# Performance work log

Hardware: AMD Instinct MI355X
Metric: run time of the kernel (lower is better)

Reference implementation:

```python
import jax, jax.numpy as jnp
import numpy as np

B, T, S, H, V, MAXL = 8, 128, 256, 1024, 32000, 512
STD = 0.02


def _ln(x, g, b):
    m = jnp.mean(x, -1, keepdims=True)
    v = jnp.mean((x - m) ** 2, -1, keepdims=True)
    return (x - m) / jnp.sqrt(v + 1e-5) * g + b


def setup_inputs() -> dict:
    key = jax.random.key(0)
    ks = jax.random.split(key, 16)
    n = lambda k, shape: jax.random.normal(k, shape, jnp.float32) * STD
    inp = {
        "input_ids": jax.random.randint(ks[0], (B, T), 0, V),
        "encoder_hidden_states": jax.random.normal(ks[1], (B, S, H), jnp.float32),
        "pattern_masks": jax.random.randint(ks[2], (B, T, V), 0, 2).astype(bool),
        "attention_mask": jnp.ones((B, S), bool),
        "tok_emb": n(ks[3], (V, H)),
        "pos_emb": n(ks[4], (MAXL, H)),
        "w_ih": n(ks[5], (4 * H, H)),
        "w_hh": n(ks[6], (4 * H, H)),
        "b_ih": jnp.zeros((4 * H,), jnp.float32),
        "b_hh": jnp.zeros((4 * H,), jnp.float32),
        "wq": n(ks[7], (H, H)), "bq": jnp.zeros((H,), jnp.float32),
        "wk": n(ks[8], (H, H)), "bk": jnp.zeros((H,), jnp.float32),
        "wc": n(ks[9], (H, 2 * H)), "bc": jnp.zeros((H,), jnp.float32),
        "wo": n(ks[10], (V, H)), "bo": jnp.zeros((V,), jnp.float32),
        "g1": n(ks[11], (H,)), "be1": jnp.zeros((H,), jnp.float32),
        "g2": n(ks[12], (H,)), "be2": jnp.zeros((H,), jnp.float32),
    }
    return inp


def reference(input_ids, encoder_hidden_states, pattern_masks, attention_mask,
              tok_emb, pos_emb, w_ih, w_hh, b_ih, b_hh,
              wq, bq, wk, bk, wc, bc, wo, bo, g1, be1, g2, be2):
    # Token + positional embedding (dropout is identity in eval)
    x = tok_emb[input_ids] + pos_emb[:T][None, :, :]  # [B,T,H]

    # Single-layer LSTM (PyTorch gate order i,f,g,o) via scan over time
    def step(carry, xt):
        h, c = carry
        gates = xt @ w_ih.T + b_ih + h @ w_hh.T + b_hh
        i, f, g, o = jnp.split(gates, 4, axis=-1)
        c = jax.nn.sigmoid(f) * c + jax.nn.sigmoid(i) * jnp.tanh(g)
        h = jax.nn.sigmoid(o) * jnp.tanh(c)
        return (h, c), h

    h0 = jnp.zeros((B, H), x.dtype)
    _, hs = jax.lax.scan(step, (h0, h0), jnp.swapaxes(x, 0, 1))
    lstm_out = jnp.swapaxes(hs, 0, 1)  # [B,T,H]

    # Attention: per-position loop in torch == batched over T (keys invariant)
    qn = _ln(lstm_out @ wq.T + bq, g1, be1)              # [B,T,H]
    kn = _ln(encoder_hidden_states @ wk.T + bk, g1, be1)  # [B,S,H]
    scale = H ** (-0.5) * 0.5
    scores = jnp.einsum('bth,bsh->bts', qn, kn) * scale
    am = attention_mask[:, None, :]
    scores = jnp.where(am, scores, -10000.0)
    mx = jnp.max(scores, -1, keepdims=True)
    ex = jnp.exp(scores - mx)
    ex = jnp.where(am, ex, 0.0)
    w = ex / (jnp.sum(ex, -1, keepdims=True) + 1e-6)
    ctx = jnp.einsum('bts,bsh->bth', w, kn)              # [B,T,H]

    hidden = _ln(jnp.concatenate([lstm_out, ctx], -1) @ wc.T + bc, g2, be2)
    logits = hidden @ wo.T + bo                           # [B,T,V]
    logits = jnp.where(pattern_masks, logits, -10000.0)
    return logits
```

## Files before the change

### kernel.cpp

```cpp
#include <hip/hip_runtime.h>
#include <cstdint>
#include <cstddef>

#define Bdim 8
#define Tdim 128
#define Sdim 256
#define Hdim 1024
#define Vdim 32000
#define SENT 0xFFFFFFFFFFFFFFFFULL

typedef unsigned short u16;
typedef unsigned long long u64;
typedef __attribute__((ext_vector_type(8))) short short8;
typedef __attribute__((ext_vector_type(4))) short short4v;
typedef __attribute__((ext_vector_type(4))) float f32x4;
typedef __attribute__((ext_vector_type(2))) unsigned long long u64x2;

union Frag { short8 v; short4v h[2]; };

__device__ __forceinline__ float bf2f(u16 u){
  union { unsigned int i; float f; } x; x.i = ((unsigned int)u) << 16; return x.f;
}
__device__ __forceinline__ u16 f2b(float f){
  union { float f; unsigned int u; } x; x.f = f;
  unsigned int r = x.u + 0x7FFFu + ((x.u >> 16) & 1u);
  return (u16)(r >> 16);
}
__device__ __forceinline__ float ftanh(float x){
  x = fminf(10.f, fmaxf(-10.f, x));
  const float e = __expf(2.f * x);
  return (e - 1.f) / (e + 1.f);
}

__device__ __forceinline__ void gload16(const void* g, void* l){
  __builtin_amdgcn_global_load_lds((const __attribute__((address_space(1))) unsigned int*)g,
                                   (__attribute__((address_space(3))) unsigned int*)l, 16, 0, 0);
}

__device__ __forceinline__ int qsw(int r){ return (r + (r >> 2)) & 3; }

__device__ __forceinline__ u64 aload(const u64* p){
  return __hip_atomic_load(p, __ATOMIC_RELAXED, __HIP_MEMORY_SCOPE_AGENT);
}
__device__ __forceinline__ void astore(u64* p, u64 v){
  __hip_atomic_store(p, v, __ATOMIC_RELAXED, __HIP_MEMORY_SCOPE_AGENT);
}

__global__ __launch_bounds__(256) void detect_bool_k(const unsigned char* __restrict__ p, int* __restrict__ flag){
  __shared__ int s;
  if (threadIdx.x == 0) s = 0;
  __syncthreads();
  int loc = 0;
  for (int i = threadIdx.x; i < 65536; i += 256)
    if ((i & 3) && p[i]) loc = 1;
  if (loc) atomicOr(&s, 1);
  __syncthreads();
  if (threadIdx.x == 0) flag[0] = s;
}

__device__ __forceinline__ bool mask_at(const void* m, size_t idx, int byteflag){
  if (byteflag) return ((const unsigned char*)m)[idx] != 0;
  return ((const int*)m)[idx] != 0;
}

template<typename OutT, bool BF32, int MASK>
__device__ __forceinline__ void gemm_core(
    char* ldsA0, char* ldsB0, char* ldsA1, char* ldsB1,
    int m0, int n0, int z,
    const u16* __restrict__ A, int lda, long sA,
    const void* __restrict__ Bp, int ldb, long sB,
    OutT* __restrict__ C, int ldc, long sC,
    const float* __restrict__ bias,
    const void* __restrict__ mask,
    const int* __restrict__ mflag,
    int K, float alpha)
{
  const int tid  = threadIdx.x;
  const int lane = tid & 63, wid = tid >> 6;
  const int lm = lane & 15, lg = lane >> 4;
  const int wm = wid >> 1, wn = wid & 1;
  const char* Ab = (const char*)(A + (size_t)z * sA);

  f32x4 acc[4][4];
#pragma unroll
  for (int i = 0; i < 4; i++)
#pragma unroll
    for (int j = 0; j < 4; j++) acc[i][j] = (f32x4){0.f, 0.f, 0.f, 0.f};

  const int brow = tid >> 1, bhalf = tid & 1;
  const int qb_st = qsw(brow);

  auto stageA = [&](char* dst, int k0){
    const char* ga = Ab + ((size_t)m0 * lda + k0) * 2;
    const int f0 = tid, f1 = tid + 256;
    const int r0 = f0 >> 2, r1 = f1 >> 2;
    gload16(ga + (size_t)r0 * (lda * 2) + ((f0 & 3) ^ qsw(r0)) * 16, dst + (f0 & ~63) * 16);
    gload16(ga + (size_t)r1 * (lda * 2) + ((f1 & 3) ^ qsw(r1)) * 16, dst + (f1 & ~63) * 16);
  };
  auto stageB16 = [&](char* dst, int k0){
    const char* gb = (const char*)((const u16*)Bp + (size_t)z * sB) + ((size_t)n0 * ldb + k0) * 2;
    const int f0 = tid, f1 = tid + 256;
    const int r0 = f0 >> 2, r1 = f1 >> 2;
    gload16(gb + (size_t)r0 * (ldb * 2) + ((f0 & 3) ^ qsw(r0)) * 16, dst + (f0 & ~63) * 16);
    gload16(gb + (size_t)r1 * (ldb * 2) + ((f1 & 3) ^ qsw(r1)) * 16, dst + (f1 & ~63) * 16);
  };

  float4 nv0, nv1, nv2, nv3;
  auto loadB32 = [&](int k0){
    const float* Bf = (const float*)Bp + (size_t)z * sB;
    const float4* src = (const float4*)(Bf + (size_t)(n0 + brow) * ldb + k0 + bhalf * 16);
    nv0 = src[0]; nv1 = src[1]; nv2 = src[2]; nv3 = src[3];
  };
  auto writeB32 = [&](char* dst){
    union { short8 v; short s[8]; } p0, p1;
    p0.s[0]=(short)f2b(nv0.x); p0.s[1]=(short)f2b(nv0.y); p0.s[2]=(short)f2b(nv0.z); p0.s[3]=(short)f2b(nv0.w);
    p0.s[4]=(short)f2b(nv1.x); p0.s[5]=(short)f2b(nv1.y); p0.s[6]=(short)f2b(nv1.z); p0.s[7]=(short)f2b(nv1.w);
    p1.s[0]=(short)f2b(nv2.x); p1.s[1]=(short)f2b(nv2.y); p1.s[2]=(short)f2b(nv2.z); p1.s[3]=(short)f2b(nv2.w);
    p1.s[4]=(short)f2b(nv3.x); p1.s[5]=(short)f2b(nv3.y); p1.s[6]=(short)f2b(nv3.z); p1.s[7]=(short)f2b(nv3.w);
    char* base = dst + brow * 64;
    *(short8*)(base + (((bhalf * 2 + 0) ^ qb_st) * 16)) = p0.v;
    *(short8*)(base + (((bhalf * 2 + 1) ^ qb_st) * 16)) = p1.v;
  };

  stageA(ldsA0, 0);
  if (BF32) { loadB32(0); writeB32(ldsB0); }
  else stageB16(ldsB0, 0);
  __syncthreads();

  char *cA = ldsA0, *cB = ldsB0, *nA = ldsA1, *nB = ldsB1;
  const int nk = K >> 5;
  for (int i = 0; i < nk; i++) {
    const bool more = (i + 1) < nk;
    if (more) {
      stageA(nA, (i + 1) << 5);
      if (BF32) loadB32((i + 1) << 5);
      else stageB16(nB, (i + 1) << 5);
    }
    Frag a[4], b[4];
#pragma unroll
    for (int mi = 0; mi < 4; mi++) {
      const int rr = wm * 64 + mi * 16 + lm;
      const int q = qsw(rr);
      const char* p = cA + rr * 64 + (lg & 1) * 8;
      a[mi].h[0] = *(const short4v*)(p + (((lg >> 1) ^ q) * 16));
      a[mi].h[1] = *(const short4v*)(p + ((((lg >> 1) | 2) ^ q) * 16));
    }
#pragma unroll
    for (int ni = 0; ni < 4; ni++) {
      const int rr = wn * 64 + ni * 16 + lm;
      const int q = qsw(rr);
      const char* p = cB + rr * 64 + (lg & 1) * 8;
      b[ni].h[0] = *(const short4v*)(p + (((lg >> 1) ^ q) * 16));
      b[ni].h[1] = *(const short4v*)(p + ((((lg >> 1) | 2) ^ q) * 16));
    }
#pragma unroll
    for (int mi = 0; mi < 4; mi++)
#pragma unroll
      for (int ni = 0; ni < 4; ni++)
        acc[mi][ni] = __builtin_amdgcn_mfma_f32_16x16x32_bf16(a[mi].v, b[ni].v, acc[mi][ni], 0, 0, 0);
    if (BF32 && more) writeB32(nB);
    __syncthreads();
    char* t;
    t = cA; cA = nA; nA = t;
    t = cB; cB = nB; nB = t;
  }

  const int bflag = (MASK == 1) ? *mflag : 0;
#pragma unroll
  for (int mi = 0; mi < 4; mi++) {
#pragma unroll
    for (int ni = 0; ni < 4; ni++) {
      const int row = m0 + wm * 64 + mi * 16 + lg * 4;
      const int col = n0 + wn * 64 + ni * 16 + lm;
      const float bb = bias ? bias[col] : 0.f;
#pragma unroll
      for (int j = 0; j < 4; j++) {
        float v = acc[mi][ni][j] * alpha + bb;
        const size_t midx = (size_t)(row + j) * ldc + col;
        if (MASK == 1) { if (!mask_at(mask, midx, bflag)) v = -10000.0f; }
        if (MASK == 2) { if (!((const unsigned char*)mask)[midx]) v = -10000.0f; }
        const size_t o = (size_t)z * sC + midx;
        if constexpr (sizeof(OutT) == 2) C[o] = (OutT)f2b(v); else C[o] = (OutT)v;
      }
    }
  }
}

template<typename OutT, bool BF32, int MASK, bool SWAP>
__global__ __launch_bounds__(256) void gemm_bt(
    const u16* __restrict__ A, int lda, long sA,
    const void* __restrict__ Bp, int ldb, long sB,
    OutT* __restrict__ C, int ldc, long sC,
    const float* __restrict__ bias,
    const void* __restrict__ mask,
    const int* __restrict__ mflag,
    int K, float alpha)
{
  __shared__ alignas(16) char lds[32768];
  const int m0 = (SWAP ? blockIdx.x : blockIdx.y) * 128;
  const int n0 = (SWAP ? blockIdx.y : blockIdx.x) * 128;
  gemm_core<OutT, BF32, MASK>(lds, lds + 8192, lds + 16384, lds + 24576,
      m0, n0, blockIdx.z, A, lda, sA, Bp, ldb, sB, C, ldc, sC,
      bias, mask, mflag, K, alpha);
}

__device__ void lstm_body(char* smem,
    const u16* __restrict__ xpre, const u16* __restrict__ whh,
    u16* __restrict__ hbuf, int bx)
{
  u16* wlds = (u16*)smem;
  u16* hlds = (u16*)(smem + 131072);
  float* g_lds = (float*)(smem + 147456);
  u16* hout = (u16*)(smem + 149632);
  const int tid = threadIdx.x, lane = tid & 63, wid = tid >> 6;
  const int lm = lane & 15, lg = lane >> 4;
  const int gcol0 = bx * 64;

  for (int q = tid; q < 8192; q += 256) {
    const int r = q >> 7, cc = q & 127;
    gload16(whh + (size_t)(gcol0 + r) * 1024 + (size_t)(cc ^ (r & 7)) * 8,
            (char*)wlds + (q & ~63) * 16);
  }

  float c_reg = 0.f;
  const int m_u = lane & 7, u_u = lane >> 3;
  const int rloc = wid * 16 + lm, swb = rloc & 7, swa = lm & 7;
  const u16* wl = wlds + rloc * 1024;
  const u16* hl = hlds + swa * 1024;
  const int gcol = gcol0 + wid * 16 + lm;
  const int pk = tid >> 2, qq = tid & 3;

  for (int t = 0; t < Tdim; t++) {
    u16 xv[4];
#pragma unroll
    for (int j = 0; j < 4; j++) {
      const int m = lg * 4 + j;
      xv[j] = (m < 8) ? xpre[(size_t)(m * Tdim + t) * 4096 + gcol] : (u16)0;
    }
    if (t > 0) {
      const u64* ps = (const u64*)(hbuf + ((size_t)(t - 1) * 64 + pk) * 128) + qq * 8;
      u64 w0=SENT,w1=SENT,w2=SENT,w3=SENT,w4=SENT,w5=SENT,w6=SENT,w7=SENT;
      for (;;) {
        if (w0 == SENT) w0 = aload(ps + 0);
        if (w1 == SENT) w1 = aload(ps + 1);
        if (w2 == SENT) w2 = aload(ps + 2);
        if (w3 == SENT) w3 = aload(ps + 3);
        if (w4 == SENT) w4 = aload(ps + 4);
        if (w5 == SENT) w5 = aload(ps + 5);
        if (w6 == SENT) w6 = aload(ps + 6);
        if (w7 == SENT) w7 = aload(ps + 7);
        if (w0 != SENT && w1 != SENT && w2 != SENT && w3 != SENT &&
            w4 != SENT && w5 != SENT && w6 != SENT && w7 != SENT) break;
        __builtin_amdgcn_s_sleep(1);
      }
      {
        const int m = qq * 2;
        u64x2 a; a[0] = w0; a[1] = w1;
        u64x2 b; b[0] = w2; b[1] = w3;
        *(u64x2*)((char*)hlds + m * 2048 + (((pk * 2 + 0) ^ m) * 16)) = a;
        *(u64x2*)((char*)hlds + m * 2048 + (((pk * 2 + 1) ^ m) * 16)) = b;
      }
      {
        const int m = qq * 2 + 1;
        u64x2 a; a[0] = w4; a[1] = w5;
        u64x2 b; b[0] = w6; b[1] = w7;
        *(u64x2*)((char*)hlds + m * 2048 + (((pk * 2 + 0) ^ m) * 16)) = a;
        *(u64x2*)((char*)hlds + m * 2048 + (((pk * 2 + 1) ^ m) * 16)) = b;
      }
    }
    __syncthreads();

    f32x4 acc;
#pragma unroll
    for (int j = 0; j < 4; j++) acc[j] = bf2f(xv[j]);

    if (t > 0) {
#pragma unroll 4
      for (int kk = 0; kk < 32; kk++) {
        const int c0 = kk * 4 + (lg >> 1);
        const int sub = (lg & 1) * 4;
        Frag a, b;
        a.h[0] = *(const short4v*)(hl + ((c0 ^ swa) << 3) + sub);
        a.h[1] = *(const short4v*)(hl + (((c0 + 2) ^ swa) << 3) + sub);
        b.h[0] = *(const short4v*)(wl + ((c0 ^ swb) << 3) + sub);
        b.h[1] = *(const short4v*)(wl + (((c0 + 2) ^ swb) << 3) + sub);
        acc = __builtin_amdgcn_mfma_f32_16x16x32_bf16(a.v, b.v, acc, 0, 0, 0);
      }
    }
#pragma unroll
    for (int j = 0; j < 4; j++) {
      const int m = lg * 4 + j;
      if (m < 8) g_lds[(wid * 8 + m) * 17 + lm] = acc[j];
    }
    __syncthreads();
    if (lane < 32) {
      const float gi = g_lds[(wid * 8 + m_u) * 17 + u_u * 4 + 0];
      const float gf = g_lds[(wid * 8 + m_u) * 17 + u_u * 4 + 1];
      const float gg = g_lds[(wid * 8 + m_u) * 17 + u_u * 4 + 2];
      const float go = g_lds[(wid * 8 + m_u) * 17 + u_u * 4 + 3];
      const float si = 1.f / (1.f + __expf(-gi));
      const float sf = 1.f / (1.f + __expf(-gf));
      const float so = 1.f / (1.f + __expf(-go));
      const float cn = sf * c_reg + si * ftanh(gg);
      c_reg = cn;
      const float hn = so * ftanh(cn);
      hout[m_u * 16 + wid * 4 + u_u] = f2b(hn);
    }
    __syncthreads();
    if (tid < 16) {
      const int m = tid >> 1, half = tid & 1;
      const u64* src = (const u64*)(hout + m * 16 + half * 8);
      u64* dst = (u64*)(hbuf + ((size_t)t * 64 + bx) * 128 + m * 16 + half * 8);
      astore(dst, src[0]);
      astore(dst + 1, src[1]);
    }
  }
}

__global__ __launch_bounds__(256) void lstm_plus(
    const u16* __restrict__ xpre, const u16* __restrict__ whh,
    u16* __restrict__ hbuf,
    const u16* __restrict__ encb, const u16* __restrict__ wkb,
    float* __restrict__ klin, const float* __restrict__ bk,
    const float* __restrict__ wo, u16* __restrict__ wob,
    const void* __restrict__ pmask, unsigned char* __restrict__ pmaskb,
    const int* __restrict__ bflag)
{
  __shared__ alignas(16) char smem[149888];
  const int bx = blockIdx.x;
  if (bx < 64) {
    lstm_body(smem, xpre, whh, hbuf, bx);
  } else if (bx < 192) {
    const int idx = bx - 64;
    gemm_core<float, false, 0>(smem, smem + 8192, smem + 16384, smem + 24576,
        (idx >> 3) * 128, (idx & 7) * 128, 0,
        encb, 1024, 0, wkb, 1024, 0, klin, 1024, 0, bk, nullptr, nullptr, 1024, 1.f);
  } else {
    const int s = bx - 192;
    const int tid = threadIdx.x;
    if (wob) {
      for (int r = s; r < Vdim; r += 64) {
        const size_t i = (size_t)r * 1024 + tid * 4;
        const float4 v = *(const float4*)(wo + i);
        u16* op = wob + i;
        op[0] = f2b(v.x); op[1] = f2b(v.y); op[2] = f2b(v.z); op[3] = f2b(v.w);
      }
    }
    if (pmaskb) {
      const int bfl = *bflag;
      const size_t total = (size_t)Bdim * Tdim * Vdim;
      const size_t nthr = 64 * 256;
      if (bfl == 0) {
        for (size_t i = ((size_t)s * 256 + tid) * 4; i < total; i += nthr * 4) {
          const int4 v = *(const int4*)((const int*)pmask + i);
          uchar4 o;
          o.x = v.x ? 1 : 0; o.y = v.y ? 1 : 0; o.z = v.z ? 1 : 0; o.w = v.w ? 1 : 0;
          *(uchar4*)(pmaskb + i) = o;
        }
      } else {
        for (size_t i = ((size_t)s * 256 + tid) * 16; i < total; i += nthr * 16) {
          *(int4*)(pmaskb + i) = *(const int4*)((const unsigned char*)pmask + i);
        }
      }
    }
  }
}

__global__ __launch_bounds__(256) void hbuf_cat_k(const u16* __restrict__ hbuf, u16* __restrict__ cat){
  const int t = blockIdx.x, tid = threadIdx.x;
  const int p = tid >> 2, q = tid & 3;
  const u64* src = (const u64*)(hbuf + ((size_t)t * 64 + p) * 128);
#pragma unroll
  for (int m = 0; m < 8; m++) {
    const u64 v = src[m * 4 + q];
    *(u64*)(cat + (size_t)(m * Tdim + t) * 2048 + p * 16 + q * 4) = v;
  }
}

__global__ __launch_bounds__(256) void prep_k(
    const float* __restrict__ w_hh, const float* __restrict__ w_ih,
    const float* __restrict__ wq,   const float* __restrict__ wk,
    const float* __restrict__ wc,   const float* __restrict__ enc,
    const int* __restrict__ ids,
    const float* __restrict__ tok,  const float* __restrict__ pos,
    const float* __restrict__ b_ih, const float* __restrict__ b_hh,
    u16* __restrict__ whhb, u16* __restrict__ wihb,
    u16* __restrict__ wqb,  u16* __restrict__ wkb,  u16* __restrict__ wcb,
    u16* __restrict__ encb, u16* __restrict__ xbf,
    float* __restrict__ biasf, u64* __restrict__ hbuf)
{
  const int b = blockIdx.x, tid = threadIdx.x;
  if (b < 8192) {
    const bool ih = b >= 4096;
    const int r = b & 4095;
    const int p = (r & 3) * Hdim + (r >> 2);
    const float4 v = *(const float4*)((ih ? w_ih : w_hh) + (size_t)p * Hdim + tid * 4);
    u16* op = (ih ? wihb : whhb) + (size_t)r * Hdim + tid * 4;
    op[0] = f2b(v.x); op[1] = f2b(v.y); op[2] = f2b(v.z); op[3] = f2b(v.w);
  } else if (b < 9216) {
    const size_t i = (size_t)(b - 8192) * 1024 + tid * 4;
    const float4 v = *(const float4*)(wq + i);
    u16* op = wqb + i;
    op[0] = f2b(v.x); op[1] = f2b(v.y); op[2] = f2b(v.z); op[3] = f2b(v.w);
  } else if (b < 10240) {
    const size_t i = (size_t)(b - 9216) * 1024 + tid * 4;
    const float4 v = *(const float4*)(wk + i);
    u16* op = wkb + i;
    op[0] = f2b(v.x); op[1] = f2b(v.y); op[2] = f2b(v.z); op[3] = f2b(v.w);
  } else if (b < 12288) {
    const size_t i = (size_t)(b - 10240) * 1024 + tid * 4;
    const float4 v = *(const float4*)(wc + i);
    u16* op = wcb + i;
    op[0] = f2b(v.x); op[1] = f2b(v.y); op[2] = f2b(v.z); op[3] = f2b(v.w);
  } else if (b < 14336) {
    const size_t i = (size_t)(b - 12288) * 1024 + tid * 4;
    const float4 v = *(const float4*)(enc + i);
    u16* op = encb + i;
    op[0] = f2b(v.x); op[1] = f2b(v.y); op[2] = f2b(v.z); op[3] = f2b(v.w);
  } else if (b < 15360) {
    const int row = b - 14336;
    const int t = row & (Tdim - 1);
    const int id = ids[row];
    const int h0 = tid * 4;
    const float4 a = *(const float4*)(tok + (size_t)id * Hdim + h0);
    const float4 p = *(const float4*)(pos + (size_t)t * Hdim + h0);
    u16* op = xbf + (size_t)row * Hdim + h0;
    op[0] = f2b(a.x + p.x); op[1] = f2b(a.y + p.y); op[2] = f2b(a.z + p.z); op[3] = f2b(a.w + p.w);
  } else if (b < 15364) {
    const int n0 = (b - 15360) * 1024 + tid * 4;
#pragma unroll
    for (int j = 0; j < 4; j++) {
      const int n = n0 + j;
      const int p = (n & 3) * Hdim + (n >> 2);
      biasf[n] = b_ih[p] + b_hh[p];
    }
  } else {
    const size_t i = ((size_t)(b - 15364) * 256 + tid) * 4;
    u64x2 s2; s2[0] = SENT; s2[1] = SENT;
    *(u64x2*)(hbuf + i)     = s2;
    *(u64x2*)(hbuf + i + 2) = s2;
  }
}

__global__ __launch_bounds__(256) void ln_rows(const float* __restrict__ in, u16* __restrict__ out,
                                               const float* __restrict__ g, const float* __restrict__ be){
  const int row = blockIdx.x, tid = threadIdx.x;
  const int lane = tid & 63, wid = tid >> 6;
  const float4 x = *(const float4*)(in + (size_t)row * Hdim + tid * 4);
  float s = x.x + x.y + x.z + x.w;
  float q = x.x * x.x + x.y * x.y + x.z * x.z + x.w * x.w;
  for (int o = 32; o; o >>= 1) { s += __shfl_down(s, o, 64); q += __shfl_down(q, o, 64); }
  __shared__ float sm[8];
  if (lane == 0) { sm[wid] = s; sm[4 + wid] = q; }
  __syncthreads();
  const float ts = sm[0] + sm[1] + sm[2] + sm[3];
  const float tq = sm[4] + sm[5] + sm[6] + sm[7];
  const float mean = ts * (1.f / Hdim);
  const float var  = tq * (1.f / Hdim) - mean * mean;
  const float r = rsqrtf(var + 1e-5f);
  const int h0 = tid * 4;
  const float4 gv = *(const float4*)(g + h0);
  const float4 bv = *(const float4*)(be + h0);
  u16* op = out + (size_t)row * Hdim + h0;
  op[0] = f2b((x.x - mean) * r * gv.x + bv.x);
  op[1] = f2b((x.y - mean) * r * gv.y + bv.y);
  op[2] = f2b((x.z - mean) * r * gv.z + bv.z);
  op[3] = f2b((x.w - mean) * r * gv.w + bv.w);
}
__global__ __launch_bounds__(256) void softmax_k(const float* __restrict__ sc, const void* __restrict__ am,
                                                 const int* __restrict__ mflag, u16* __restrict__ w){
  const int row = blockIdx.x, tid = threadIdx.x;
  const int lane = tid & 63, wid = tid >> 6;
  const int b = row >> 7;
  const int bflag = *mflag;
  const float v = sc[(size_t)row * Sdim + tid];
  const bool mk = mask_at(am, (size_t)b * Sdim + tid, bflag);
  const float vm = mk ? v : -10000.0f;
  float mx = vm;
  for (int o = 32; o; o >>= 1) mx = fmaxf(mx, __shfl_down(mx, o, 64));
  __shared__ float sm[8];
  if (lane == 0) sm[wid] = mx;
  __syncthreads();
  mx = fmaxf(fmaxf(sm[0], sm[1]), fmaxf(sm[2], sm[3]));
  const float ex = mk ? expf(vm - mx) : 0.f;
  float ss = ex;
  for (int o = 32; o; o >>= 1) ss += __shfl_down(ss, o, 64);
  if (lane == 0) sm[4 + wid] = ss;
  __syncthreads();
  const float tot = sm[4] + sm[5] + sm[6] + sm[7];
  w[(size_t)row * Sdim + tid] = f2b(ex / (tot + 1e-6f));
}
__global__ __launch_bounds__(256) void transp_k(const u16* __restrict__ kn, u16* __restrict__ knT){
  __shared__ u16 tile[64][65];
  const int b = blockIdx.z, h0 = blockIdx.x * 64, s0 = blockIdx.y * 64;
  const u16* src = kn  + (size_t)b * Sdim * Hdim;
  u16* dst       = knT + (size_t)b * Hdim * Sdim;
  for (int e = threadIdx.x; e < 4096; e += 256) {
    const int r = e >> 6, c = e & 63;
    tile[r][c] = src[(size_t)(s0 + r) * Hdim + h0 + c];
  }
  __syncthreads();
  for (int e = threadIdx.x; e < 4096; e += 256) {
    const int hr = e >> 6, scc = e & 63;
    dst[(size_t)(h0 + hr) * Sdim + s0 + scc] = tile[scc][hr];
  }
}

extern "C" void kernel_launch(void* const* d_in, const int* in_sizes, int n_in,
                              void* d_out, int out_size, void* d_ws, size_t ws_size,
                              hipStream_t stream) {
  const int*   input_ids = (const int*)d_in[0];
  const float* enc   = (const float*)d_in[1];
  const void*  pmask = d_in[2];
  const void*  amask = d_in[3];
  const float* tok  = (const float*)d_in[4];
  const float* pos  = (const float*)d_in[5];
  const float* w_ih = (const float*)d_in[6];
  const float* w_hh = (const float*)d_in[7];
  const float* b_ih = (const float*)d_in[8];
  const float* b_hh = (const float*)d_in[9];
  const float* wq = (const float*)d_in[10];
  const float* bq = (const float*)d_in[11];
  const float* wk = (const float*)d_in[12];
  const float* bk = (const float*)d_in[13];
  const float* wc = (const float*)d_in[14];
  const float* bc = (const float*)d_in[15];
  const float* wo = (const float*)d_in[16];
  const float* bo = (const float*)d_in[17];
  const float* g1  = (const float*)d_in[18];
  const float* be1 = (const float*)d_in[19];
  const float* g2  = (const float*)d_in[20];
  const float* be2 = (const float*)d_in[21];
  float* out = (float*)d_out;

  char* ws = (char*)d_ws;
  size_t off = 0;
  auto alloc = [&](size_t b){ size_t o = off; off += (b + 255) & ~(size_t)255; return o; };
  u16*   whhb  = (u16*)  (ws + alloc((size_t)4096 * 1024 * 2));
  u16*   wihb  = (u16*)  (ws + alloc((size_t)4096 * 1024 * 2));
  u16*   wqb   = (u16*)  (ws + alloc((size_t)1024 * 1024 * 2));
  u16*   wkb   = (u16*)  (ws + alloc((size_t)1024 * 1024 * 2));
  u16*   wcb   = (u16*)  (ws + alloc((size_t)1024 * 2048 * 2));
  float* biasf = (float*)(ws + alloc(4096 * 4));
  u16*   xbf   = (u16*)  (ws + alloc((size_t)1024 * 1024 * 2));
  u16*   encb  = (u16*)  (ws + alloc((size_t)2048 * 1024 * 2));
  u16*   xpre  = (u16*)  (ws + alloc((size_t)1024 * 4096 * 2));
  u16*   hbuf  = (u16*)  (ws + alloc((size_t)Tdim * 64 * 128 * 2));
  u16*   cat   = (u16*)  (ws + alloc((size_t)1024 * 2048 * 2));
  float* qlin  = (float*)(ws + alloc((size_t)1024 * 1024 * 4));
  u16*   qn    = (u16*)  (ws + alloc((size_t)1024 * 1024 * 2));
  float* klin  = (float*)(ws + alloc((size_t)2048 * 1024 * 4));
  u16*   kn    = (u16*)  (ws + alloc((size_t)2048 * 1024 * 2));
  u16*   knT   = (u16*)  (ws + alloc((size_t)2048 * 1024 * 2));
  float* scores= (float*)(ws + alloc((size_t)8 * 128 * 256 * 4));
  u16*   attw  = (u16*)  (ws + alloc((size_t)8 * 128 * 256 * 2));
  float* hlin  = (float*)(ws + alloc((size_t)1024 * 1024 * 4));
  u16*   hid   = (u16*)  (ws + alloc((size_t)1024 * 1024 * 2));
  int*   bflag = (int*)  (ws + alloc(256));
  unsigned char* pmaskb = (unsigned char*)(ws + alloc((size_t)Bdim * Tdim * Vdim));
  const bool havePak = off <= ws_size;
  u16*   wob   = (u16*)  (ws + alloc((size_t)Vdim * Hdim * 2));
  const bool haveWob = off <= ws_size;
  if (!havePak) pmaskb = nullptr;
  if (!haveWob) wob = nullptr;
  (void)in_sizes; (void)n_in; (void)out_size;

  detect_bool_k<<<1, 256, 0, stream>>>((const unsigned char*)pmask, bflag);
  prep_k<<<15620, 256, 0, stream>>>(w_hh, w_ih, wq, wk, wc, enc, input_ids,
      tok, pos, b_ih, b_hh, whhb, wihb, wqb, wkb, wcb, encb, xbf, biasf, (u64*)hbuf);

  gemm_bt<u16, false, 0, false><<<dim3(32, 8, 1), 256, 0, stream>>>(
      xbf, 1024, 0, wihb, 1024, 0, xpre, 4096, 0, biasf, nullptr, nullptr, 1024, 1.f);

  lstm_plus<<<256, 256, 0, stream>>>(xpre, whhb, hbuf, encb, wkb, klin, bk,
                                     wo, wob, pmask, pmaskb, bflag);
  hbuf_cat_k<<<Tdim, 256, 0, stream>>>(hbuf, cat);

  gemm_bt<float, false, 0, false><<<dim3(8, 8, 1), 256, 0, stream>>>(
      cat, 2048, 0, wqb, 1024, 0, qlin, 1024, 0, bq, nullptr, nullptr, 1024, 1.f);
  ln_rows<<<1024, 256, 0, stream>>>(qlin, qn, g1, be1);
  ln_rows<<<2048, 256, 0, stream>>>(klin, kn, g1, be1);
  transp_k<<<dim3(16, 4, 8), 256, 0, stream>>>(kn, knT);

  gemm_bt<float, false, 0, false><<<dim3(2, 1, 8), 256, 0, stream>>>(
      qn, 1024, 131072, kn, 1024, 262144, scores, 256, 32768, nullptr, nullptr, nullptr, 1024, 0.015625f);
  softmax_k<<<1024, 256, 0, stream>>>(scores, amask, bflag, attw);
  gemm_bt<u16, false, 0, false><<<dim3(8, 1, 8), 256, 0, stream>>>(
      attw, 256, 32768, knT, 256, 262144, cat + 1024, 2048, 262144, nullptr, nullptr, nullptr, 256, 1.f);

  gemm_bt<float, false, 0, false><<<dim3(8, 8, 1), 256, 0, stream>>>(
      cat, 2048, 0, wcb, 2048, 0, hlin, 1024, 0, bc, nullptr, nullptr, 2048, 1.f);
  ln_rows<<<1024, 256, 0, stream>>>(hlin, hid, g2, be2);

  if (wob && pmaskb)
    gemm_bt<float, false, 2, true><<<dim3(8, 250, 1), 256, 0, stream>>>(
        hid, 1024, 0, wob, 1024, 0, out, 32000, 0, bo, pmaskb, nullptr, 1024, 1.f);
  else if (wob)
    gemm_bt<float, false, 1, true><<<dim3(8, 250, 1), 256, 0, stream>>>(
        hid, 1024, 0, wob, 1024, 0, out, 32000, 0, bo, pmask, bflag, 1024, 1.f);
  else
    gemm_bt<float, true, 1, true><<<dim3(8, 250, 1), 256, 0, stream>>>(
        hid, 1024, 0, wo, 1024, 0, out, 32000, 0, bo, pmask, bflag, 1024, 1.f);
}
```

Before: 957.8 us.

## Swap MFMA operands in LSTM step to keep gates in registers, drop LDS round-trips

The recurrent LSTM step now puts the weights in the A operand and h in the B operand, so each lane ends up holding all four gates for one (batch, unit) pair. The gate nonlinearities are then computed directly in registers, replacing two LDS staging passes and two __syncthreads per timestep with a few cross-lane shuffles and a direct packed store of h. The K loop is fully unrolled and split over four independent accumulators to break the MFMA dependency chain, and the x pre-activation load becomes one vectorized 8-byte load. This targets the serial per-timestep latency of the LSTM chain, at the cost of more registers and redundant activation math in lanes whose results are discarded.

```diff
diff --git a/kernel.cpp b/kernel.cpp
--- a/kernel.cpp
+++ b/kernel.cpp
@@ -210,8 +210,6 @@
 {
   u16* wlds = (u16*)smem;
   u16* hlds = (u16*)(smem + 131072);
-  float* g_lds = (float*)(smem + 147456);
-  u16* hout = (u16*)(smem + 149632);
   const int tid = threadIdx.x, lane = tid & 63, wid = tid >> 6;
   const int lm = lane & 15, lg = lane >> 4;
   const int gcol0 = bx * 64;
@@ -223,20 +221,15 @@
   }
 
   float c_reg = 0.f;
-  const int m_u = lane & 7, u_u = lane >> 3;
   const int rloc = wid * 16 + lm, swb = rloc & 7, swa = lm & 7;
   const u16* wl = wlds + rloc * 1024;
   const u16* hl = hlds + swa * 1024;
-  const int gcol = gcol0 + wid * 16 + lm;
   const int pk = tid >> 2, qq = tid & 3;
+  const u16* xp = xpre + (size_t)(lm * Tdim) * 4096 + gcol0 + wid * 16 + lg * 4;
 
   for (int t = 0; t < Tdim; t++) {
-    u16 xv[4];
-#pragma unroll
-    for (int j = 0; j < 4; j++) {
-      const int m = lg * 4 + j;
-      xv[j] = (m < 8) ? xpre[(size_t)(m * Tdim + t) * 4096 + gcol] : (u16)0;
-    }
+    u64 xw = 0;
+    if (lm < 8) xw = *(const u64*)(xp + (size_t)t * 4096);
     if (t > 0) {
       const u64* ps = (const u64*)(hbuf + ((size_t)(t - 1) * 64 + pk) * 128) + qq * 8;
       u64 w0=SENT,w1=SENT,w2=SENT,w3=SENT,w4=SENT,w5=SENT,w6=SENT,w7=SENT;
@@ -270,50 +263,52 @@
     }
     __syncthreads();
 
-    f32x4 acc;
-#pragma unroll
-    for (int j = 0; j < 4; j++) acc[j] = bf2f(xv[j]);
+    f32x4 acc0, acc1, acc2, acc3;
+    {
+      union { u64 w; u16 s[4]; } xu; xu.w = xw;
+      acc0[0] = bf2f(xu.s[0]); acc0[1] = bf2f(xu.s[1]);
+      acc0[2] = bf2f(xu.s[2]); acc0[3] = bf2f(xu.s[3]);
+    }
+    acc1 = (f32x4){0.f,0.f,0.f,0.f};
+    acc2 = (f32x4){0.f,0.f,0.f,0.f};
+    acc3 = (f32x4){0.f,0.f,0.f,0.f};
 
     if (t > 0) {
-#pragma unroll 4
+#pragma unroll
       for (int kk = 0; kk < 32; kk++) {
         const int c0 = kk * 4 + (lg >> 1);
         const int sub = (lg & 1) * 4;
-        Frag a, b;
-        a.h[0] = *(const short4v*)(hl + ((c0 ^ swa) << 3) + sub);
-        a.h[1] = *(const short4v*)(hl + (((c0 + 2) ^ swa) << 3) + sub);
-        b.h[0] = *(const short4v*)(wl + ((c0 ^ swb) << 3) + sub);
-        b.h[1] = *(const short4v*)(wl + (((c0 + 2) ^ swb) << 3) + sub);
-        acc = __builtin_amdgcn_mfma_f32_16x16x32_bf16(a.v, b.v, acc, 0, 0, 0);
-      }
-    }
-#pragma unroll
-    for (int j = 0; j < 4; j++) {
-      const int m = lg * 4 + j;
-      if (m < 8) g_lds[(wid * 8 + m) * 17 + lm] = acc[j];
+        Frag aw, bh;
+        aw.h[0] = *(const short4v*)(wl + ((c0 ^ swb) << 3) + sub);
+        aw.h[1] = *(const short4v*)(wl + (((c0 + 2) ^ swb) << 3) + sub);
+        bh.h[0] = *(const short4v*)(hl + ((c0 ^ swa) << 3) + sub);
+        bh.h[1] = *(const short4v*)(hl + (((c0 + 2) ^ swa) << 3) + sub);
+        if ((kk & 3) == 0)      acc0 = __builtin_amdgcn_mfma_f32_16x16x32_bf16(aw.v, bh.v, acc0, 0, 0, 0);
+        else if ((kk & 3) == 1) acc1 = __builtin_amdgcn_mfma_f32_16x16x32_bf16(aw.v, bh.v, acc1, 0, 0, 0);
+        else if ((kk & 3) == 2) acc2 = __builtin_amdgcn_mfma_f32_16x16x32_bf16(aw.v, bh.v, acc2, 0, 0, 0);
+        else                    acc3 = __builtin_amdgcn_mfma_f32_16x16x32_bf16(aw.v, bh.v, acc3, 0, 0, 0);
+      }
+    }
+    const f32x4 g4 = (acc0 + acc1) + (acc2 + acc3);
+
+    const float si = 1.f / (1.f + __expf(-g4[0]));
+    const float sf = 1.f / (1.f + __expf(-g4[1]));
+    const float so = 1.f / (1.f + __expf(-g4[3]));
+    const float cn = sf * c_reg + si * ftanh(g4[2]);
+    c_reg = cn;
+    const float hn = so * ftanh(cn);
+    const int hb = (int)f2b(hn);
+
+    const int v0 = __shfl(hb, lm, 64);
+    const int v1 = __shfl(hb, lm + 16, 64);
+    const int v2 = __shfl(hb, lm + 32, 64);
+    const int v3 = __shfl(hb, lm + 48, 64);
+    if (lg == 0 && lm < 8) {
+      const u64 pack = (u64)(v0 & 0xFFFF) | ((u64)(v1 & 0xFFFF) << 16)
+                     | ((u64)(v2 & 0xFFFF) << 32) | ((u64)(v3 & 0xFFFF) << 48);
+      astore((u64*)(hbuf + ((size_t)t * 64 + bx) * 128 + lm * 16 + wid * 4), pack);
     }
     __syncthreads();
-    if (lane < 32) {
-      const float gi = g_lds[(wid * 8 + m_u) * 17 + u_u * 4 + 0];
-      const float gf = g_lds[(wid * 8 + m_u) * 17 + u_u * 4 + 1];
-      const float gg = g_lds[(wid * 8 + m_u) * 17 + u_u * 4 + 2];
-      const float go = g_lds[(wid * 8 + m_u) * 17 + u_u * 4 + 3];
-      const float si = 1.f / (1.f + __expf(-gi));
-      const float sf = 1.f / (1.f + __expf(-gf));
-      const float so = 1.f / (1.f + __expf(-go));
-      const float cn = sf * c_reg + si * ftanh(gg);
-      c_reg = cn;
-      const float hn = so * ftanh(cn);
-      hout[m_u * 16 + wid * 4 + u_u] = f2b(hn);
-    }
-    __syncthreads();
-    if (tid < 16) {
-      const int m = tid >> 1, half = tid & 1;
-      const u64* src = (const u64*)(hout + m * 16 + half * 8);
-      u64* dst = (u64*)(hbuf + ((size_t)t * 64 + bx) * 128 + m * 16 + half * 8);
-      astore(dst, src[0]);
-      astore(dst + 1, src[1]);
-    }
   }
 }
 
@@ -326,7 +321,7 @@
     const void* __restrict__ pmask, unsigned char* __restrict__ pmaskb,
     const int* __restrict__ bflag)
 {
-  __shared__ alignas(16) char smem[149888];
+  __shared__ alignas(16) char smem[147456];
   const int bx = blockIdx.x;
   if (bx < 64) {
     lstm_body(smem, xpre, whh, hbuf, bx);
```

New measurement: 801.7 us. 16.3% less time.
